# Performance work log

Hardware: AMD Instinct MI355X
Metric: run time of the kernel (lower is better)

The kernel has to match this reference:

```python
import jax, jax.numpy as jnp
import numpy as np

B, NPG, D_IN, D, L = 64, 512, 1, 128, 10
N = B * NPG
DEG = 16
E = N * DEG
EPS = 1e-5


def setup_inputs() -> dict:
    key = jax.random.key(0)
    ks = jax.random.split(key, 8)
    x = jax.random.normal(ks[0], (N, D_IN), jnp.float32)
    # edges confined within each graph: local indices + per-graph offset
    src_local = jax.random.randint(ks[1], (E,), 0, NPG)
    dst_local = jax.random.randint(ks[2], (E,), 0, NPG)
    offs = (jnp.arange(E) // (E // B)) * NPG
    edge_src = (src_local + offs).astype(jnp.int32)
    edge_dst = (dst_local + offs).astype(jnp.int32)
    batch = jnp.repeat(jnp.arange(B, dtype=jnp.int32), NPG)
    g = lambda k, s, fan: jax.random.normal(k, s, jnp.float32) / np.float32(np.sqrt(fan))
    W0 = g(ks[3], (D_IN, D), D_IN)
    b0 = jnp.zeros((D,), jnp.float32)
    W_rest = g(ks[4], (L - 1, D, D), D)
    b_rest = jnp.zeros((L - 1, D), jnp.float32)
    gamma = jnp.ones((L, D), jnp.float32)
    beta = jnp.zeros((L, D), jnp.float32)
    W_att = g(ks[5], (D, D), D)
    return dict(x=x, edge_src=edge_src, edge_dst=edge_dst, batch=batch,
                W0=W0, b0=b0, W_rest=W_rest, b_rest=b_rest,
                gamma=gamma, beta=beta, W_att=W_att)


def _gcn_conv(h, W, b, src, dst, norm_e, self_w):
    # GCNConv: h' = D^-1/2 (A + I) D^-1/2 (h W) + b  (symmetric norm, self-loops)
    h = h @ W
    msg = norm_e[:, None] * h[src]                      # [E, D] gather
    agg = jax.ops.segment_sum(msg, dst, num_segments=N)  # [N, D] scatter-add
    return agg + self_w[:, None] * h + b


def _bn_relu(h, g, b):
    mu = jnp.mean(h, axis=0)
    var = jnp.var(h, axis=0)
    return jax.nn.relu(g * (h - mu) * jax.lax.rsqrt(var + EPS) + b)


def reference(x, edge_src, edge_dst, batch, W0, b0, W_rest, b_rest, gamma, beta, W_att):
    # symmetric GCN normalization with self-loops (edge weight 1)
    deg = 1.0 + jax.ops.segment_sum(jnp.ones((E,), x.dtype), edge_dst, num_segments=N)
    dinv = jax.lax.rsqrt(deg)
    norm_e = dinv[edge_src] * dinv[edge_dst]   # [E]
    self_w = dinv * dinv                        # [N] self-loop coefficient

    h = _gcn_conv(x, W0, b0, edge_src, edge_dst, norm_e, self_w)
    h = _bn_relu(h, gamma[0], beta[0])
    for l in range(L - 1):
        h = _gcn_conv(h, W_rest[l], b_rest[l], edge_src, edge_dst, norm_e, self_w)
        h = _bn_relu(h, gamma[l + 1], beta[l + 1])

    # graph attention pooling
    mean = jax.ops.segment_sum(h, batch, num_segments=B) / jnp.float32(NPG)  # [B, D]
    tg = jnp.tanh(mean @ W_att)                                              # [B, D]
    coefs = jax.nn.sigmoid(jnp.sum(h * tg[batch], axis=1) * 10.0)            # [N]
    graph_feat = jax.ops.segment_sum(coefs[:, None] * h, batch, num_segments=B)  # [B, D]

    # to_dense_batch (equal-sized graphs -> exact reshape) + concat broadcast graph feat
    node_dense = h.reshape(B, NPG, D)
    gf = jnp.broadcast_to(graph_feat[:, None, :], (B, NPG, D))
    return jnp.concatenate([node_dense, gf], axis=-1)  # [B, NPG, 2D]
```

## Files before the change

kernel.cpp:

```cpp
#include <hip/hip_runtime.h>
#include <hip/hip_bf16.h>
#include <math.h>

#define NN 32768
#define BG 64
#define NPGC 512
#define DD 128
#define EE 524288
#define LL 10
#define EPSF 1e-5f
#define PADK 72

typedef __attribute__((ext_vector_type(8))) short short8;
typedef __attribute__((ext_vector_type(4))) float float4v;

static __device__ __forceinline__ unsigned short f2bf(float x) {
    __hip_bfloat16 b = __float2bfloat16(x);
    return *reinterpret_cast<unsigned short*>(&b);
}
static __device__ __forceinline__ float bf2f(unsigned short u) {
    unsigned int v = ((unsigned int)u) << 16;
    return __uint_as_float(v);
}
static __device__ __forceinline__ void splitbf(float x, unsigned short& h, unsigned short& l) {
    unsigned short hh = f2bf(x);
    h = hh;
    l = f2bf(x - bf2f(hh));
}


__global__ void k_histM(const int* __restrict__ src, const int* __restrict__ dst,
                        int* __restrict__ Mint, int* __restrict__ cnt) {
    int e = blockIdx.x * 256 + threadIdx.x;
    int d = dst[e], s = src[e] & 511;
    atomicAdd(&Mint[(size_t)d * 512 + s], 1);
    atomicAdd(&cnt[d], 1);
}

__global__ void k_dinv(const int* __restrict__ cnt, float* __restrict__ dinv) {
    int n = blockIdx.x * 256 + threadIdx.x;
    dinv[n] = rsqrtf(1.0f + (float)cnt[n]);
}

__global__ void k_conv(const int* __restrict__ Mint, unsigned short* __restrict__ Mh) {
    int idx = (blockIdx.x * 256 + threadIdx.x) * 4;
    int4 v = *(const int4*)(Mint + idx);
    int row = idx >> 9;
    int diag = row & 511;
    int cb = idx & 511;
    unsigned short us[4];
    us[0] = f2bf((float)(v.x + (cb + 0 == diag ? 1 : 0)));
    us[1] = f2bf((float)(v.y + (cb + 1 == diag ? 1 : 0)));
    us[2] = f2bf((float)(v.z + (cb + 2 == diag ? 1 : 0)));
    us[3] = f2bf((float)(v.w + (cb + 3 == diag ? 1 : 0)));
    *(uint2*)(Mh + idx) = *(uint2*)us;
}

__global__ void k_wt(const float* __restrict__ Wr, unsigned short* __restrict__ Wt_h,
                     unsigned short* __restrict__ Wt_l) {
    int idx = blockIdx.x * 256 + threadIdx.x;
    int l = idx >> 14, rem = idx & 16383;
    int fp = rem >> 7, f = rem & 127;
    unsigned short h, lo;
    splitbf(Wr[l * 16384 + f * 128 + fp], h, lo);
    Wt_h[idx] = h;
    Wt_l[idx] = lo;
}

__global__ void k_l0(const float* __restrict__ x, const float* __restrict__ W0,
                     const float* __restrict__ dinv,
                     unsigned short* __restrict__ hwT_h, unsigned short* __restrict__ hwT_l) {
    int u = blockIdx.x * 256 + threadIdx.x;
    int f = u >> 12, n0 = (u & 4095) * 8;
    float w = W0[f];
    float4 xa = *(const float4*)(x + n0);
    float4 xb = *(const float4*)(x + n0 + 4);
    float4 da = *(const float4*)(dinv + n0);
    float4 db = *(const float4*)(dinv + n0 + 4);
    float v[8] = {xa.x * w * da.x, xa.y * w * da.y, xa.z * w * da.z, xa.w * w * da.w,
                  xb.x * w * db.x, xb.y * w * db.y, xb.z * w * db.z, xb.w * w * db.w};
    unsigned short uh[8], ul[8];
    #pragma unroll
    for (int i = 0; i < 8; i++) splitbf(v[i], uh[i], ul[i]);
    *(uint4*)(hwT_h + (size_t)f * NN + n0) = *(uint4*)uh;
    *(uint4*)(hwT_l + (size_t)f * NN + n0) = *(uint4*)ul;
}

__global__ __launch_bounds__(256) void k_aggmm(const unsigned short* __restrict__ Mh,
        const unsigned short* __restrict__ hwT_h, const unsigned short* __restrict__ hwT_l,
        const float* __restrict__ dinv, const float* __restrict__ bias,
        float* __restrict__ pre, float* __restrict__ stats) {
    __shared__ unsigned short As[64 * PADK];
    __shared__ unsigned short Bs_h[128 * PADK], Bs_l[128 * PADK];
    int t = threadIdx.x, lane = t & 63, wv = t >> 6;
    int l15 = lane & 15, quad = lane >> 4;
    int b = blockIdx.x, r = b & 7, q = b >> 3;
    int g = r + 8 * (q & 7);
    int mb = (q >> 3) * 64;
    size_t arow = ((size_t)g * 512 + mb) * 512;
    size_t gcol = (size_t)g * 512;
    float4v acc[8];
    #pragma unroll
    for (int i = 0; i < 8; i++) acc[i] = (float4v)0.f;

    for (int kc = 0; kc < 512; kc += 64) {
        __syncthreads();
        #pragma unroll
        for (int i = 0; i < 2; i++) {
            int u = t + i * 256;
            int row = u >> 3, ko = (u & 7) * 8;
            *(uint4*)(&As[row * PADK + ko]) =
                *(const uint4*)(Mh + arow + (size_t)row * 512 + kc + ko);
        }
        #pragma unroll
        for (int i = 0; i < 4; i++) {
            int u = t + i * 256;
            int f = u >> 3, ko = (u & 7) * 8;
            size_t go = (size_t)f * NN + gcol + kc + ko;
            *(uint4*)(&Bs_h[f * PADK + ko]) = *(const uint4*)(hwT_h + go);
            *(uint4*)(&Bs_l[f * PADK + ko]) = *(const uint4*)(hwT_l + go);
        }
        __syncthreads();
        int f0 = wv * 32;
        #pragma unroll
        for (int ks = 0; ks < 2; ks++) {
            int kb = ks * 32 + quad * 8;
            short8 a0 = *(const short8*)(&As[(l15) * PADK + kb]);
            short8 a1 = *(const short8*)(&As[(16 + l15) * PADK + kb]);
            short8 a2 = *(const short8*)(&As[(32 + l15) * PADK + kb]);
            short8 a3 = *(const short8*)(&As[(48 + l15) * PADK + kb]);
            #pragma unroll
            for (int nt = 0; nt < 2; nt++) {
                short8 bh = *(const short8*)(&Bs_h[(f0 + nt * 16 + l15) * PADK + kb]);
                short8 bl = *(const short8*)(&Bs_l[(f0 + nt * 16 + l15) * PADK + kb]);
                acc[0 + nt] = __builtin_amdgcn_mfma_f32_16x16x32_bf16(a0, bh, acc[0 + nt], 0, 0, 0);
                acc[0 + nt] = __builtin_amdgcn_mfma_f32_16x16x32_bf16(a0, bl, acc[0 + nt], 0, 0, 0);
                acc[2 + nt] = __builtin_amdgcn_mfma_f32_16x16x32_bf16(a1, bh, acc[2 + nt], 0, 0, 0);
                acc[2 + nt] = __builtin_amdgcn_mfma_f32_16x16x32_bf16(a1, bl, acc[2 + nt], 0, 0, 0);
                acc[4 + nt] = __builtin_amdgcn_mfma_f32_16x16x32_bf16(a2, bh, acc[4 + nt], 0, 0, 0);
                acc[4 + nt] = __builtin_amdgcn_mfma_f32_16x16x32_bf16(a2, bl, acc[4 + nt], 0, 0, 0);
                acc[6 + nt] = __builtin_amdgcn_mfma_f32_16x16x32_bf16(a3, bh, acc[6 + nt], 0, 0, 0);
                acc[6 + nt] = __builtin_amdgcn_mfma_f32_16x16x32_bf16(a3, bl, acc[6 + nt], 0, 0, 0);
            }
        }
    }
    int gbase = g * 512 + mb;
    #pragma unroll
    for (int nt = 0; nt < 2; nt++) {
        int f = wv * 32 + nt * 16 + l15;
        float bf = bias[f];
        float cs = 0.f, cq = 0.f;
        #pragma unroll
        for (int mt = 0; mt < 4; mt++) {
            int n0 = gbase + mt * 16 + quad * 4;
            float4 dv = *(const float4*)(dinv + n0);
            float4v a = acc[mt * 2 + nt];
            float v0 = fmaf(dv.x, a[0], bf);
            float v1 = fmaf(dv.y, a[1], bf);
            float v2 = fmaf(dv.z, a[2], bf);
            float v3 = fmaf(dv.w, a[3], bf);
            pre[(size_t)(n0 + 0) * 128 + f] = v0;
            pre[(size_t)(n0 + 1) * 128 + f] = v1;
            pre[(size_t)(n0 + 2) * 128 + f] = v2;
            pre[(size_t)(n0 + 3) * 128 + f] = v3;
            cs += v0 + v1 + v2 + v3;
            cq = fmaf(v0, v0, cq); cq = fmaf(v1, v1, cq);
            cq = fmaf(v2, v2, cq); cq = fmaf(v3, v3, cq);
        }
        cs += __shfl_xor(cs, 16); cs += __shfl_xor(cs, 32);
        cq += __shfl_xor(cq, 16); cq += __shfl_xor(cq, 32);
        if (quad == 0) {
            atomicAdd(&stats[f], cs);
            atomicAdd(&stats[128 + f], cq);
        }
    }
}

__global__ __launch_bounds__(256) void k_mmT(const float* __restrict__ pre,
        const float* __restrict__ stats, const float* __restrict__ gamma,
        const float* __restrict__ beta, const float* __restrict__ dinv,
        const unsigned short* __restrict__ Wt_h, const unsigned short* __restrict__ Wt_l,
        unsigned short* __restrict__ hwT_h, unsigned short* __restrict__ hwT_l) {
    __shared__ unsigned short Ws_h[128 * PADK], Ws_l[128 * PADK];
    __shared__ unsigned short Xs_h[64 * PADK], Xs_l[64 * PADK];
    __shared__ float scL[256];
    int t = threadIdx.x, lane = t & 63, wv = t >> 6;
    int l15 = lane & 15, quad = lane >> 4;
    int b = blockIdx.x, r = b & 7, q = b >> 3;
    int g = r + 8 * (q & 7);
    int nb = g * NPGC + (q >> 3) * 64;
    if (t < 128) {
        float mu = stats[t] * (1.0f / NN);
        float var = stats[128 + t] * (1.0f / NN) - mu * mu;
        float s = gamma[t] * rsqrtf(var + EPSF);
        scL[t] = s;
        scL[128 + t] = fmaf(-mu, s, beta[t]);
    }
    float4v acc[8];
    #pragma unroll
    for (int i = 0; i < 8; i++) acc[i] = (float4v)0.f;

    for (int kc = 0; kc < 128; kc += 64) {
        __syncthreads();
        #pragma unroll
        for (int i = 0; i < 4; i++) {
            int u = t + i * 256;
            int fp = u >> 3, ko = (u & 7) * 8;
            int go = fp * 128 + kc + ko;
            *(uint4*)(&Ws_h[fp * PADK + ko]) = *(const uint4*)(Wt_h + go);
            *(uint4*)(&Ws_l[fp * PADK + ko]) = *(const uint4*)(Wt_l + go);
        }
        #pragma unroll
        for (int i = 0; i < 2; i++) {
            int u = t + i * 256;
            int n = u >> 3, fo = (u & 7) * 8;
            const float* pp = pre + (size_t)(nb + n) * 128 + kc + fo;
            float4 v0 = *(const float4*)(pp);
            float4 v1 = *(const float4*)(pp + 4);
            float4 s0 = *(const float4*)(&scL[kc + fo]);
            float4 s1 = *(const float4*)(&scL[kc + fo + 4]);
            float4 h0 = *(const float4*)(&scL[128 + kc + fo]);
            float4 h1 = *(const float4*)(&scL[128 + kc + fo + 4]);
            float v[8] = {fmaxf(fmaf(v0.x, s0.x, h0.x), 0.f),
                          fmaxf(fmaf(v0.y, s0.y, h0.y), 0.f),
                          fmaxf(fmaf(v0.z, s0.z, h0.z), 0.f),
                          fmaxf(fmaf(v0.w, s0.w, h0.w), 0.f),
                          fmaxf(fmaf(v1.x, s1.x, h1.x), 0.f),
                          fmaxf(fmaf(v1.y, s1.y, h1.y), 0.f),
                          fmaxf(fmaf(v1.z, s1.z, h1.z), 0.f),
                          fmaxf(fmaf(v1.w, s1.w, h1.w), 0.f)};
            unsigned short uh[8], ul[8];
            #pragma unroll
            for (int j = 0; j < 8; j++) splitbf(v[j], uh[j], ul[j]);
            *(uint4*)(&Xs_h[n * PADK + fo]) = *(uint4*)uh;
            *(uint4*)(&Xs_l[n * PADK + fo]) = *(uint4*)ul;
        }
        __syncthreads();
        int m0 = wv * 32;
        #pragma unroll
        for (int ks = 0; ks < 2; ks++) {
            int kb = ks * 32 + quad * 8;
            short8 a0h = *(const short8*)(&Ws_h[(m0 + l15) * PADK + kb]);
            short8 a0l = *(const short8*)(&Ws_l[(m0 + l15) * PADK + kb]);
            short8 a1h = *(const short8*)(&Ws_h[(m0 + 16 + l15) * PADK + kb]);
            short8 a1l = *(const short8*)(&Ws_l[(m0 + 16 + l15) * PADK + kb]);
            #pragma unroll
            for (int nt = 0; nt < 4; nt++) {
                short8 bh = *(const short8*)(&Xs_h[(nt * 16 + l15) * PADK + kb]);
                short8 bl = *(const short8*)(&Xs_l[(nt * 16 + l15) * PADK + kb]);
                acc[nt]     = __builtin_amdgcn_mfma_f32_16x16x32_bf16(a0h, bh, acc[nt], 0, 0, 0);
                acc[nt]     = __builtin_amdgcn_mfma_f32_16x16x32_bf16(a0h, bl, acc[nt], 0, 0, 0);
                acc[nt]     = __builtin_amdgcn_mfma_f32_16x16x32_bf16(a0l, bh, acc[nt], 0, 0, 0);
                acc[4 + nt] = __builtin_amdgcn_mfma_f32_16x16x32_bf16(a1h, bh, acc[4 + nt], 0, 0, 0);
                acc[4 + nt] = __builtin_amdgcn_mfma_f32_16x16x32_bf16(a1h, bl, acc[4 + nt], 0, 0, 0);
                acc[4 + nt] = __builtin_amdgcn_mfma_f32_16x16x32_bf16(a1l, bh, acc[4 + nt], 0, 0, 0);
            }
        }
    }
    #pragma unroll
    for (int mt = 0; mt < 2; mt++) {
        #pragma unroll
        for (int nt = 0; nt < 4; nt++) {
            int n = nb + nt * 16 + l15;
            float dv = dinv[n];
            int fp0 = wv * 32 + mt * 16 + quad * 4;
            float4v a = acc[mt * 4 + nt];
            #pragma unroll
            for (int rg = 0; rg < 4; rg++) {
                unsigned short h, lo;
                splitbf(dv * a[rg], h, lo);
                hwT_h[(size_t)(fp0 + rg) * NN + n] = h;
                hwT_l[(size_t)(fp0 + rg) * NN + n] = lo;
            }
        }
    }
}

__global__ __launch_bounds__(256) void k_bn_pool(float* __restrict__ pre,
        const float* __restrict__ stats, const float* __restrict__ gamma,
        const float* __restrict__ beta, float* __restrict__ meansum) {
    __shared__ float ssum[256];
    __shared__ float scL[256];
    int t = threadIdx.x;
    int b = blockIdx.x, r = b & 7, q = b >> 3;
    int g = r + 8 * (q & 7);
    int nb = g * NPGC + (q >> 3) * 64;
    if (t < 128) {
        float mu = stats[t] * (1.0f / NN);
        float var = stats[128 + t] * (1.0f / NN) - mu * mu;
        float s = gamma[t] * rsqrtf(var + EPSF);
        scL[t] = s;
        scL[128 + t] = fmaf(-mu, s, beta[t]);
    }
    __syncthreads();
    int f = t & 127;
    float s = scL[f], sh = scL[128 + f];
    float lsum = 0.f;
    int base = nb * 128;
    for (int i = 0; i < 32; i++) {
        int idx = base + i * 256 + t;
        float v = fmaxf(fmaf(pre[idx], s, sh), 0.f);
        pre[idx] = v;
        lsum += v;
    }
    ssum[t] = lsum;
    __syncthreads();
    if (t < 128) atomicAdd(&meansum[g * 128 + f], ssum[t] + ssum[t + 128]);
}

__global__ void k_tg(const float* __restrict__ meansum, const float* __restrict__ Watt,
                     float* __restrict__ tg) {
    __shared__ float m[128];
    int g = blockIdx.x, t = threadIdx.x;
    m[t] = meansum[g * 128 + t] * (1.0f / NPGC);
    __syncthreads();
    float a2 = 0.f;
    for (int k = 0; k < 128; k++) a2 = fmaf(m[k], Watt[k * 128 + t], a2);
    tg[g * 128 + t] = tanhf(a2);
}

__global__ __launch_bounds__(256) void k_coef_gf(const float* __restrict__ h,
        const float* __restrict__ tg, float* __restrict__ gf) {
    __shared__ float tgs[128];
    __shared__ float coef[64];
    int t = threadIdx.x;
    int b = blockIdx.x, r = b & 7, q = b >> 3;
    int g = r + 8 * (q & 7);
    int n0 = (q >> 3) * 64;
    if (t < 128) tgs[t] = tg[g * 128 + t];
    __syncthreads();
    int wid = t >> 6, lane = t & 63;
    const float* hp = h + (size_t)g * NPGC * 128;
    for (int j = wid; j < 64; j += 4) {
        int n = n0 + j;
        float p = hp[n * 128 + lane] * tgs[lane] + hp[n * 128 + 64 + lane] * tgs[64 + lane];
        for (int off = 32; off; off >>= 1) p += __shfl_xor(p, off);
        if (lane == 0) coef[j] = 1.0f / (1.0f + expf(-10.0f * p));
    }
    __syncthreads();
    int f = t & 127, half = t >> 7;
    float acc = 0.f;
    for (int j = 0; j < 32; j++) {
        int jj = half * 32 + j;
        acc = fmaf(coef[jj], hp[(n0 + jj) * 128 + f], acc);
    }
    atomicAdd(&gf[g * 128 + f], acc);
}

__global__ void k_out(const float* __restrict__ h, const float* __restrict__ gf,
                      float* __restrict__ out) {
    int idx = blockIdx.x * 256 + threadIdx.x;
    int c4 = (idx & 63) * 4;
    int n = idx >> 6;
    int g = n >> 9;
    float4 v = (c4 < 128) ? *(const float4*)(h + (size_t)n * 128 + c4)
                          : *(const float4*)(gf + g * 128 + (c4 - 128));
    *(float4*)(out + (size_t)idx * 4) = v;
}

extern "C" void kernel_launch(void* const* d_in, const int* in_sizes, int n_in,
                              void* d_out, int out_size, void* d_ws, size_t ws_size,
                              hipStream_t stream) {
    const float* x     = (const float*)d_in[0];
    const int*   esrc  = (const int*)d_in[1];
    const int*   edst  = (const int*)d_in[2];
    const float* W0    = (const float*)d_in[4];
    const float* b0    = (const float*)d_in[5];
    const float* Wr    = (const float*)d_in[6];
    const float* br    = (const float*)d_in[7];
    const float* gamma = (const float*)d_in[8];
    const float* beta  = (const float*)d_in[9];
    const float* Watt  = (const float*)d_in[10];
    float* out = (float*)d_out;
    float* ws  = (float*)d_ws;

    int*   cnt     = (int*)(ws + 0);
    float* dinv    = ws + 32768;
    float* stats   = ws + 65536;
    float* tgbuf   = ws + 68096;
    float* meansum = ws + 76288;
    float* gf      = ws + 84480;
    unsigned short* Wt_h  = (unsigned short*)(ws + 92672);
    unsigned short* Wt_l  = (unsigned short*)(ws + 166400);
    unsigned short* hwT_h = (unsigned short*)(ws + 240128);
    unsigned short* hwT_l = (unsigned short*)(ws + 2337280);
    unsigned short* Mh    = (unsigned short*)(ws + 4434432);
    int*   Mint    = (int*)(ws + 12823040);
    float* pre     = ws + 12823040;

    hipMemsetAsync(cnt, 0, NN * sizeof(int), stream);
    hipMemsetAsync(stats, 0, LL * 256 * sizeof(float), stream);
    hipMemsetAsync(meansum, 0, BG * 128 * sizeof(float), stream);
    hipMemsetAsync(gf, 0, BG * 128 * sizeof(float), stream);
    hipMemsetAsync(Mint, 0, (size_t)NN * 512 * sizeof(int), stream);

    k_histM<<<EE / 256, 256, 0, stream>>>(esrc, edst, Mint, cnt);
    k_dinv<<<NN / 256, 256, 0, stream>>>(cnt, dinv);
    k_conv<<<NN * 512 / 1024, 256, 0, stream>>>(Mint, Mh);
    k_wt<<<9 * 16384 / 256, 256, 0, stream>>>(Wr, Wt_h, Wt_l);
    k_l0<<<128 * (NN / 8) / 256, 256, 0, stream>>>(x, W0, dinv, hwT_h, hwT_l);

    for (int l = 0; l < LL; l++) {
        const float* bias = (l == 0) ? b0 : br + (l - 1) * DD;
        k_aggmm<<<NN / 64, 256, 0, stream>>>(Mh, hwT_h, hwT_l, dinv, bias,
                                             pre, stats + l * 256);
        if (l < LL - 1)
            k_mmT<<<NN / 64, 256, 0, stream>>>(pre, stats + l * 256, gamma + l * DD,
                                               beta + l * DD, dinv, Wt_h + l * 16384,
                                               Wt_l + l * 16384, hwT_h, hwT_l);
        else
            k_bn_pool<<<NN / 64, 256, 0, stream>>>(pre, stats + l * 256, gamma + l * DD,
                                                   beta + l * DD, meansum);
    }
    k_tg<<<BG, 128, 0, stream>>>(meansum, Watt, tgbuf);
    k_coef_gf<<<NN / 64, 256, 0, stream>>>(pre, tgbuf, gf);
    k_out<<<NN * 64 / 256, 256, 0, stream>>>(pre, gf, out);
}
```

Baseline: 538.9 us.

## Pack adjacency counts into 16-bit pairs and double aggmm row tile

After: 520.9 us. 3.3% less time.

```diff
diff --git a/kernel.cpp b/kernel.cpp
--- a/kernel.cpp
+++ b/kernel.cpp
@@ -30,10 +30,11 @@
 
 
 __global__ void k_histM(const int* __restrict__ src, const int* __restrict__ dst,
-                        int* __restrict__ Mint, int* __restrict__ cnt) {
+                        unsigned int* __restrict__ Mp, int* __restrict__ cnt) {
     int e = blockIdx.x * 256 + threadIdx.x;
     int d = dst[e], s = src[e] & 511;
-    atomicAdd(&Mint[(size_t)d * 512 + s], 1);
+    int cell = (d << 9) + s;
+    atomicAdd(&Mp[cell >> 1], 1u << ((cell & 1) << 4));
     atomicAdd(&cnt[d], 1);
 }
 
@@ -42,18 +43,18 @@
     dinv[n] = rsqrtf(1.0f + (float)cnt[n]);
 }
 
-__global__ void k_conv(const int* __restrict__ Mint, unsigned short* __restrict__ Mh) {
-    int idx = (blockIdx.x * 256 + threadIdx.x) * 4;
-    int4 v = *(const int4*)(Mint + idx);
-    int row = idx >> 9;
-    int diag = row & 511;
+__global__ void k_conv(const unsigned int* __restrict__ Mp, unsigned short* __restrict__ Mh) {
+    int idx = (blockIdx.x * 256 + threadIdx.x) * 8;
+    uint4 v = *(const uint4*)(Mp + (idx >> 1));
+    unsigned int c[8] = {v.x & 0xffffu, v.x >> 16, v.y & 0xffffu, v.y >> 16,
+                         v.z & 0xffffu, v.z >> 16, v.w & 0xffffu, v.w >> 16};
+    int diag = (idx >> 9) & 511;
     int cb = idx & 511;
-    unsigned short us[4];
-    us[0] = f2bf((float)(v.x + (cb + 0 == diag ? 1 : 0)));
-    us[1] = f2bf((float)(v.y + (cb + 1 == diag ? 1 : 0)));
-    us[2] = f2bf((float)(v.z + (cb + 2 == diag ? 1 : 0)));
-    us[3] = f2bf((float)(v.w + (cb + 3 == diag ? 1 : 0)));
-    *(uint2*)(Mh + idx) = *(uint2*)us;
+    unsigned short us[8];
+    #pragma unroll
+    for (int j = 0; j < 8; j++)
+        us[j] = f2bf((float)(c[j] + ((cb + j == diag) ? 1u : 0u)));
+    *(uint4*)(Mh + idx) = *(uint4*)us;
 }
 
 __global__ void k_wt(const float* __restrict__ Wr, unsigned short* __restrict__ Wt_h,
@@ -90,23 +91,23 @@
         const unsigned short* __restrict__ hwT_h, const unsigned short* __restrict__ hwT_l,
         const float* __restrict__ dinv, const float* __restrict__ bias,
         float* __restrict__ pre, float* __restrict__ stats) {
-    __shared__ unsigned short As[64 * PADK];
+    __shared__ unsigned short As[128 * PADK];
     __shared__ unsigned short Bs_h[128 * PADK], Bs_l[128 * PADK];
     int t = threadIdx.x, lane = t & 63, wv = t >> 6;
     int l15 = lane & 15, quad = lane >> 4;
     int b = blockIdx.x, r = b & 7, q = b >> 3;
     int g = r + 8 * (q & 7);
-    int mb = (q >> 3) * 64;
+    int mb = (q >> 3) * 128;
     size_t arow = ((size_t)g * 512 + mb) * 512;
     size_t gcol = (size_t)g * 512;
-    float4v acc[8];
-    #pragma unroll
-    for (int i = 0; i < 8; i++) acc[i] = (float4v)0.f;
+    float4v acc[16];
+    #pragma unroll
+    for (int i = 0; i < 16; i++) acc[i] = (float4v)0.f;
 
     for (int kc = 0; kc < 512; kc += 64) {
         __syncthreads();
         #pragma unroll
-        for (int i = 0; i < 2; i++) {
+        for (int i = 0; i < 4; i++) {
             int u = t + i * 256;
             int row = u >> 3, ko = (u & 7) * 8;
             *(uint4*)(&As[row * PADK + ko]) =
@@ -125,35 +126,34 @@
         #pragma unroll
         for (int ks = 0; ks < 2; ks++) {
             int kb = ks * 32 + quad * 8;
-            short8 a0 = *(const short8*)(&As[(l15) * PADK + kb]);
-            short8 a1 = *(const short8*)(&As[(16 + l15) * PADK + kb]);
-            short8 a2 = *(const short8*)(&As[(32 + l15) * PADK + kb]);
-            short8 a3 = *(const short8*)(&As[(48 + l15) * PADK + kb]);
+            short8 a[8];
+            #pragma unroll
+            for (int mt = 0; mt < 8; mt++)
+                a[mt] = *(const short8*)(&As[(mt * 16 + l15) * PADK + kb]);
             #pragma unroll
             for (int nt = 0; nt < 2; nt++) {
                 short8 bh = *(const short8*)(&Bs_h[(f0 + nt * 16 + l15) * PADK + kb]);
                 short8 bl = *(const short8*)(&Bs_l[(f0 + nt * 16 + l15) * PADK + kb]);
-                acc[0 + nt] = __builtin_amdgcn_mfma_f32_16x16x32_bf16(a0, bh, acc[0 + nt], 0, 0, 0);
-                acc[0 + nt] = __builtin_amdgcn_mfma_f32_16x16x32_bf16(a0, bl, acc[0 + nt], 0, 0, 0);
-                acc[2 + nt] = __builtin_amdgcn_mfma_f32_16x16x32_bf16(a1, bh, acc[2 + nt], 0, 0, 0);
-                acc[2 + nt] = __builtin_amdgcn_mfma_f32_16x16x32_bf16(a1, bl, acc[2 + nt], 0, 0, 0);
-                acc[4 + nt] = __builtin_amdgcn_mfma_f32_16x16x32_bf16(a2, bh, acc[4 + nt], 0, 0, 0);
-                acc[4 + nt] = __builtin_amdgcn_mfma_f32_16x16x32_bf16(a2, bl, acc[4 + nt], 0, 0, 0);
-                acc[6 + nt] = __builtin_amdgcn_mfma_f32_16x16x32_bf16(a3, bh, acc[6 + nt], 0, 0, 0);
-                acc[6 + nt] = __builtin_amdgcn_mfma_f32_16x16x32_bf16(a3, bl, acc[6 + nt], 0, 0, 0);
+                #pragma unroll
+                for (int mt = 0; mt < 8; mt++) {
+                    acc[mt * 2 + nt] = __builtin_amdgcn_mfma_f32_16x16x32_bf16(a[mt], bh, acc[mt * 2 + nt], 0, 0, 0);
+                    acc[mt * 2 + nt] = __builtin_amdgcn_mfma_f32_16x16x32_bf16(a[mt], bl, acc[mt * 2 + nt], 0, 0, 0);
+                }
             }
         }
     }
     int gbase = g * 512 + mb;
-    #pragma unroll
-    for (int nt = 0; nt < 2; nt++) {
-        int f = wv * 32 + nt * 16 + l15;
-        float bf = bias[f];
-        float cs = 0.f, cq = 0.f;
-        #pragma unroll
-        for (int mt = 0; mt < 4; mt++) {
-            int n0 = gbase + mt * 16 + quad * 4;
-            float4 dv = *(const float4*)(dinv + n0);
+    int fA = wv * 32 + l15;
+    float bf0 = bias[fA], bf1 = bias[fA + 16];
+    float cs[2] = {0.f, 0.f}, cq[2] = {0.f, 0.f};
+    #pragma unroll
+    for (int mt = 0; mt < 8; mt++) {
+        int n0 = gbase + mt * 16 + quad * 4;
+        float4 dv = *(const float4*)(dinv + n0);
+        #pragma unroll
+        for (int nt = 0; nt < 2; nt++) {
+            int f = fA + nt * 16;
+            float bf = nt ? bf1 : bf0;
             float4v a = acc[mt * 2 + nt];
             float v0 = fmaf(dv.x, a[0], bf);
             float v1 = fmaf(dv.y, a[1], bf);
@@ -163,15 +163,19 @@
             pre[(size_t)(n0 + 1) * 128 + f] = v1;
             pre[(size_t)(n0 + 2) * 128 + f] = v2;
             pre[(size_t)(n0 + 3) * 128 + f] = v3;
-            cs += v0 + v1 + v2 + v3;
-            cq = fmaf(v0, v0, cq); cq = fmaf(v1, v1, cq);
-            cq = fmaf(v2, v2, cq); cq = fmaf(v3, v3, cq);
-        }
-        cs += __shfl_xor(cs, 16); cs += __shfl_xor(cs, 32);
-        cq += __shfl_xor(cq, 16); cq += __shfl_xor(cq, 32);
+            cs[nt] += v0 + v1 + v2 + v3;
+            cq[nt] = fmaf(v0, v0, cq[nt]); cq[nt] = fmaf(v1, v1, cq[nt]);
+            cq[nt] = fmaf(v2, v2, cq[nt]); cq[nt] = fmaf(v3, v3, cq[nt]);
+        }
+    }
+    #pragma unroll
+    for (int nt = 0; nt < 2; nt++) {
+        float cs_ = cs[nt], cq_ = cq[nt];
+        cs_ += __shfl_xor(cs_, 16); cs_ += __shfl_xor(cs_, 32);
+        cq_ += __shfl_xor(cq_, 16); cq_ += __shfl_xor(cq_, 32);
         if (quad == 0) {
-            atomicAdd(&stats[f], cs);
-            atomicAdd(&stats[128 + f], cq);
+            atomicAdd(&stats[fA + nt * 16], cs_);
+            atomicAdd(&stats[128 + fA + nt * 16], cq_);
         }
     }
 }
@@ -385,25 +389,25 @@
     unsigned short* hwT_h = (unsigned short*)(ws + 240128);
     unsigned short* hwT_l = (unsigned short*)(ws + 2337280);
     unsigned short* Mh    = (unsigned short*)(ws + 4434432);
-    int*   Mint    = (int*)(ws + 12823040);
+    unsigned int* Mp = (unsigned int*)(ws + 12823040);
     float* pre     = ws + 12823040;
 
     hipMemsetAsync(cnt, 0, NN * sizeof(int), stream);
     hipMemsetAsync(stats, 0, LL * 256 * sizeof(float), stream);
     hipMemsetAsync(meansum, 0, BG * 128 * sizeof(float), stream);
     hipMemsetAsync(gf, 0, BG * 128 * sizeof(float), stream);
-    hipMemsetAsync(Mint, 0, (size_t)NN * 512 * sizeof(int), stream);
-
-    k_histM<<<EE / 256, 256, 0, stream>>>(esrc, edst, Mint, cnt);
+    hipMemsetAsync(Mp, 0, (size_t)NN * 256 * sizeof(int), stream);
+
+    k_histM<<<EE / 256, 256, 0, stream>>>(esrc, edst, Mp, cnt);
     k_dinv<<<NN / 256, 256, 0, stream>>>(cnt, dinv);
-    k_conv<<<NN * 512 / 1024, 256, 0, stream>>>(Mint, Mh);
+    k_conv<<<NN * 512 / 8 / 256, 256, 0, stream>>>(Mp, Mh);
     k_wt<<<9 * 16384 / 256, 256, 0, stream>>>(Wr, Wt_h, Wt_l);
     k_l0<<<128 * (NN / 8) / 256, 256, 0, stream>>>(x, W0, dinv, hwT_h, hwT_l);
 
     for (int l = 0; l < LL; l++) {
         const float* bias = (l == 0) ? b0 : br + (l - 1) * DD;
-        k_aggmm<<<NN / 64, 256, 0, stream>>>(Mh, hwT_h, hwT_l, dinv, bias,
-                                             pre, stats + l * 256);
+        k_aggmm<<<NN / 128, 256, 0, stream>>>(Mh, hwT_h, hwT_l, dinv, bias,
+                                              pre, stats + l * 256);
         if (l < LL - 1)
             k_mmT<<<NN / 64, 256, 0, stream>>>(pre, stats + l * 256, gamma + l * DD,
                                                beta + l * DD, dinv, Wt_h + l * 16384,
```
